# Optimization experiments

Hardware: AMD Instinct MI355X
Metric: run time of the kernel (lower is better)

Reference implementation:

```python
import jax, jax.numpy as jnp
import numpy as np

NUM_HEADS = 16
MASK_NEG = -66504.0  # matches IPEX causal mask fill value


def setup_inputs() -> dict:
    key = jax.random.key(0)
    ks = jax.random.split(key, 5)
    B, S, E = 1, 2048, 2048
    return {
        "hidden_states": jax.random.normal(ks[0], (B, S, E), dtype=jnp.float32),
        "q_wei": jax.random.normal(ks[1], (E, E), dtype=jnp.float32) * (E ** -0.5),
        "k_wei": jax.random.normal(ks[2], (E, E), dtype=jnp.float32) * (E ** -0.5),
        "v_wei": jax.random.normal(ks[3], (E, E), dtype=jnp.float32) * (E ** -0.5),
        "out_wei": jax.random.normal(ks[4], (E, E), dtype=jnp.float32) * (E ** -0.5),
    }


def reference(hidden_states, q_wei, k_wei, v_wei, out_wei):
    B, S, E = hidden_states.shape
    H = NUM_HEADS
    D = E // H
    # qkv_normal (row-major path): x @ W, [B,S,E]
    q = hidden_states @ q_wei
    k = hidden_states @ k_wei
    v = hidden_states @ v_wei
    # compute_qkv view + normal_combine permute -> [B,H,S,D]
    q = q.reshape(B, S, H, D).transpose(0, 2, 1, 3)
    k = k.reshape(B, S, H, D).transpose(0, 2, 1, 3)
    v = v.reshape(B, S, H, D).transpose(0, 2, 1, 3)
    # naive_self_attention: scores, causal mask add, THEN scale divide
    scores = jnp.einsum("bhqd,bhkd->bhqk", q, k)  # [B,H,S,S]
    causal = jnp.triu(jnp.full((S, S), MASK_NEG, dtype=scores.dtype), k=1)
    scores = scores + causal[None, None]
    scores = scores / jnp.sqrt(jnp.asarray(D, dtype=scores.dtype))
    probs = jax.nn.softmax(scores.astype(jnp.float32), axis=-1).astype(q.dtype)
    attn = jnp.einsum("bhqk,bhkd->bhqd", probs, v)  # [B,H,S,D]
    # merge heads and output projection
    attn = attn.transpose(0, 2, 1, 3).reshape(B, S, E)
    return attn @ out_wei
```

## Files before the change

### kernel.cpp

```cpp
#include <hip/hip_runtime.h>

#define F16 _Float16
typedef __attribute__((ext_vector_type(8))) _Float16 half8;
typedef __attribute__((ext_vector_type(4))) _Float16 half4;
typedef __attribute__((ext_vector_type(4))) float f32x4;

constexpr int S = 2048;
constexpr int E = 2048;
constexpr float MASK_NEG = -66504.0f;
constexpr float INV_SQRT_D = 0.08838834764831845f;
constexpr float MASK_SC = MASK_NEG * INV_SQRT_D;

__device__ __forceinline__ void gload16(const void* g, void* l) {
  __builtin_amdgcn_global_load_lds((const __attribute__((address_space(1))) void*)g,
                                   (__attribute__((address_space(3))) void*)l, 16, 0, 0);
}

__global__ __launch_bounds__(256) void cast_f32_f16_k(const float* __restrict__ x,
                                                      F16* __restrict__ y) {
  size_t i = ((size_t)blockIdx.x * 256 + threadIdx.x) * 8;
  float4 a = *(const float4*)(x + i);
  float4 b = *(const float4*)(x + i + 4);
  half8 h;
  h[0] = (F16)a.x; h[1] = (F16)a.y; h[2] = (F16)a.z; h[3] = (F16)a.w;
  h[4] = (F16)b.x; h[5] = (F16)b.y; h[6] = (F16)b.z; h[7] = (F16)b.w;
  *(half8*)(y + i) = h;
}

__global__ __launch_bounds__(256) void transpose_cast2_k(const float* __restrict__ W0,
                                                         const float* __restrict__ W1,
                                                         F16* __restrict__ D0,
                                                         F16* __restrict__ D1) {
  const float* W = blockIdx.z ? W1 : W0;
  F16* Wt = blockIdx.z ? D1 : D0;
  __shared__ float tile[64][65];
  const int t = threadIdx.x;
  const int bx = blockIdx.x, by = blockIdx.y;
  {
    int r = t >> 4, c = (t & 15) << 2;
    const float* src = W + (size_t)(by * 64 + r) * E + bx * 64 + c;
    #pragma unroll
    for (int i = 0; i < 4; ++i) {
      float4 v = *(const float4*)(src + (size_t)i * 16 * E);
      tile[r + i * 16][c + 0] = v.x; tile[r + i * 16][c + 1] = v.y;
      tile[r + i * 16][c + 2] = v.z; tile[r + i * 16][c + 3] = v.w;
    }
  }
  __syncthreads();
  {
    int r = t >> 2, c = (t & 3) << 4;
    half8 v0, v1;
    #pragma unroll
    for (int i = 0; i < 8; ++i) v0[i] = (F16)tile[c + i][r];
    #pragma unroll
    for (int i = 0; i < 8; ++i) v1[i] = (F16)tile[c + 8 + i][r];
    F16* dst = Wt + (size_t)(bx * 64 + r) * E + by * 64 + c;
    *(half8*)dst = v0;
    *(half8*)(dst + 8) = v1;
  }
}

template <int MODE>
__global__ __launch_bounds__(256, 2) void gemm_bt_k(const F16* __restrict__ A,
                                                    const F16* __restrict__ Bt,
                                                    void* __restrict__ C0v,
                                                    void* __restrict__ C1v) {
  constexpr int K = 2048, N = 2048;
  __shared__ F16 sA[64 * 64];
  __shared__ F16 sB[128 * 64];
  const int t = threadIdx.x;
  const int lane = t & 63, wave = t >> 6;
  const int wr = wave >> 1, wc = wave & 1;
  const int bm = blockIdx.y, bn = blockIdx.x;

  f32x4 acc[2][4];
  #pragma unroll
  for (int mi = 0; mi < 2; ++mi)
    #pragma unroll
    for (int ni = 0; ni < 4; ++ni) acc[mi][ni] = (f32x4){0.f, 0.f, 0.f, 0.f};

  const int rb = t >> 3;
  const int bofs = (t & 7) << 4;
  const int kOff = (bofs ^ ((rb & 7) << 4)) >> 1;
  const F16* aSrc = A + (size_t)(bm * 64 + rb) * K + kOff;
  const F16* bSrc = Bt + (size_t)(bn * 128 + rb) * K + kOff;
  F16* aDst = sA + t * 8;
  F16* bDst = sB + t * 8;

  for (int bk = 0; bk < K; bk += 64) {
    #pragma unroll
    for (int it = 0; it < 2; ++it)
      gload16(aSrc + (size_t)it * 32 * K + bk, aDst + it * 2048);
    #pragma unroll
    for (int it = 0; it < 4; ++it)
      gload16(bSrc + (size_t)it * 32 * K + bk, bDst + it * 2048);
    __syncthreads();
    #pragma unroll
    for (int kk = 0; kk < 2; ++kk) {
      half8 af[2], bf[4];
      const int kb = kk * 64 + ((lane >> 4) << 4);
      #pragma unroll
      for (int i = 0; i < 2; ++i) {
        const int ra = wr * 32 + i * 16 + (lane & 15);
        af[i] = *(const half8*)((const char*)sA + ra * 128 + (kb ^ ((ra & 7) << 4)));
      }
      #pragma unroll
      for (int i = 0; i < 4; ++i) {
        const int rn = wc * 64 + i * 16 + (lane & 15);
        bf[i] = *(const half8*)((const char*)sB + rn * 128 + (kb ^ ((rn & 7) << 4)));
      }
      #pragma unroll
      for (int mi = 0; mi < 2; ++mi)
        #pragma unroll
        for (int ni = 0; ni < 4; ++ni)
          acc[mi][ni] = __builtin_amdgcn_mfma_f32_16x16x32_f16(af[mi], bf[ni], acc[mi][ni], 0, 0, 0);
    }
    __syncthreads();
  }

  const float scale = (MODE == 1 && bn < 16) ? INV_SQRT_D : 1.0f;
  void* Cv = (MODE == 1 && bn >= 16) ? C1v : C0v;
  const int cb = (MODE == 1 ? (bn & 15) : bn) * 128;

  #pragma unroll
  for (int mi = 0; mi < 2; ++mi) {
    const int r0 = bm * 64 + wr * 32 + mi * 16 + ((lane >> 4) << 2);
    #pragma unroll
    for (int ni = 0; ni < 4; ++ni) {
      const int c = cb + wc * 64 + ni * 16 + (lane & 15);
      #pragma unroll
      for (int j = 0; j < 4; ++j) {
        if (MODE == 2)
          ((float*)Cv)[(size_t)(r0 + j) * N + c] = acc[mi][ni][j];
        else
          ((F16*)Cv)[(size_t)(r0 + j) * N + c] = (F16)(acc[mi][ni][j] * scale);
      }
    }
  }
}

__global__ __launch_bounds__(256, 2) void attn_fwd_k(const F16* __restrict__ Q,
                                                     const F16* __restrict__ Km,
                                                     const F16* __restrict__ Vt,
                                                     F16* __restrict__ O) {
  __shared__ F16 sK[2][64 * 128];
  __shared__ F16 sV[2][128 * 64];
  __shared__ F16 sP[4][16 * 64];
  const int t = threadIdx.x, lane = t & 63, w = t >> 6;
  const int h = blockIdx.x & 15;
  const int bq = blockIdx.x >> 4;
  const int qt = (bq < 16) ? (31 - bq) : (bq - 16);
  const int qrow0 = qt * 64 + w * 16;
  const int g = lane >> 4;
  const int myq = qrow0 + (lane & 15);

  half8 qf[4];
  {
    const F16* qp = Q + (size_t)myq * E + h * 128 + (g << 3);
    #pragma unroll
    for (int kd = 0; kd < 4; ++kd) qf[kd] = *(const half8*)(qp + kd * 32);
  }

  f32x4 oacc[8];
  #pragma unroll
  for (int i = 0; i < 8; ++i) oacc[i] = (f32x4){0.f, 0.f, 0.f, 0.f};
  float mrun = -3e38f, lrun = 0.f;

  const int rk = t >> 4;
  const int kcol = (((t & 15) << 4) ^ ((rk & 15) << 4)) >> 1;
  const int rv = t >> 3;
  const int vcol = (((t & 7) << 4) ^ ((rv & 7) << 4)) >> 1;
  const F16* kBase = Km + (size_t)rk * E + h * 128 + kcol;
  const F16* vBase = Vt + (size_t)(h * 128 + rv) * S + vcol;
  F16* myP = (F16*)sP[w];

  auto stage = [&](int kt, int b) {
    const F16* kSrc = kBase + (size_t)kt * 64 * E;
    const F16* vSrc = vBase + kt * 64;
    #pragma unroll
    for (int it = 0; it < 4; ++it) {
      gload16(kSrc + (size_t)it * 16 * E, &sK[b][t * 8 + it * 2048]);
      gload16(vSrc + (size_t)it * 32 * S, &sV[b][t * 8 + it * 2048]);
    }
  };

  stage(0, 0);
  const int nt = qt + 1;

  for (int kt = 0; kt < nt; ++kt) {
    __syncthreads();
    if (kt + 1 < nt) stage(kt + 1, (kt + 1) & 1);
    const char* bK = (const char*)sK[kt & 1];
    const char* bV = (const char*)sV[kt & 1];

    f32x4 sacc[4];
    #pragma unroll
    for (int i = 0; i < 4; ++i) sacc[i] = (f32x4){0.f, 0.f, 0.f, 0.f};
    __builtin_amdgcn_s_setprio(1);
    #pragma unroll
    for (int kd = 0; kd < 4; ++kd) {
      const int kb = kd * 64 + (g << 4);
      #pragma unroll
      for (int ni = 0; ni < 4; ++ni) {
        const int rn = ni * 16 + (lane & 15);
        half8 kf = *(const half8*)(bK + rn * 256 + (kb ^ ((rn & 15) << 4)));
        sacc[ni] = __builtin_amdgcn_mfma_f32_16x16x32_f16(kf, qf[kd], sacc[ni], 0, 0, 0);
      }
    }
    __builtin_amdgcn_s_setprio(0);

    const bool diag = (kt == nt - 1);
    const int kv0 = kt * 64 + g * 4;
    float mx = -3e38f;
    #pragma unroll
    for (int ni = 0; ni < 4; ++ni) {
      #pragma unroll
      for (int j = 0; j < 4; ++j) {
        float s = sacc[ni][j];
        if (diag && (kv0 + ni * 16 + j) > myq) s += MASK_SC;
        sacc[ni][j] = s;
        mx = fmaxf(mx, s);
      }
    }
    mx = fmaxf(mx, __shfl_xor(mx, 16));
    mx = fmaxf(mx, __shfl_xor(mx, 32));

    if (__any(mx > mrun + 8.0f)) {
      const float mnew = fmaxf(mrun, mx);
      const float sc = __expf(mrun - mnew);
      float rs = 0.f;
      #pragma unroll
      for (int ni = 0; ni < 4; ++ni)
        #pragma unroll
        for (int j = 0; j < 4; ++j) {
          const float p = __expf(sacc[ni][j] - mnew);
          sacc[ni][j] = p;
          rs += p;
        }
      rs += __shfl_xor(rs, 16);
      rs += __shfl_xor(rs, 32);
      lrun = lrun * sc + rs;
      mrun = mnew;
      #pragma unroll
      for (int df = 0; df < 8; ++df)
        #pragma unroll
        for (int j = 0; j < 4; ++j) oacc[df][j] *= sc;
    } else {
      float rs = 0.f;
      #pragma unroll
      for (int ni = 0; ni < 4; ++ni)
        #pragma unroll
        for (int j = 0; j < 4; ++j) {
          const float p = __expf(sacc[ni][j] - mrun);
          sacc[ni][j] = p;
          rs += p;
        }
      rs += __shfl_xor(rs, 16);
      rs += __shfl_xor(rs, 32);
      lrun += rs;
    }

    {
      char* rowp = (char*)myP + (lane & 15) * 128;
      const int swz = ((lane & 15) & 7) << 4;
      #pragma unroll
      for (int ni = 0; ni < 4; ++ni) {
        half4 pk;
        #pragma unroll
        for (int j = 0; j < 4; ++j) pk[j] = (F16)sacc[ni][j];
        *(half4*)(rowp + ((ni * 32 + g * 8) ^ swz)) = pk;
      }
    }

    __builtin_amdgcn_s_setprio(1);
    #pragma unroll
    for (int kk = 0; kk < 2; ++kk) {
      const int kb = kk * 64 + (g << 4);
      const int ra = lane & 15;
      half8 pa = *(const half8*)((const char*)myP + ra * 128 + (kb ^ ((ra & 7) << 4)));
      #pragma unroll
      for (int df = 0; df < 8; ++df) {
        const int rd = df * 16 + (lane & 15);
        half8 vf = *(const half8*)(bV + rd * 128 + (kb ^ ((rd & 7) << 4)));
        oacc[df] = __builtin_amdgcn_mfma_f32_16x16x32_f16(vf, pa, oacc[df], 0, 0, 0);
      }
    }
    __builtin_amdgcn_s_setprio(0);
  }

  const float inv = 1.0f / lrun;
  F16* orow = O + (size_t)myq * E + h * 128;
  #pragma unroll
  for (int df = 0; df < 8; ++df) {
    half4 ov;
    #pragma unroll
    for (int j = 0; j < 4; ++j) ov[j] = (F16)(oacc[df][j] * inv);
    *(half4*)(orow + df * 16 + g * 4) = ov;
  }
}

extern "C" void kernel_launch(void* const* d_in, const int* in_sizes, int n_in,
                              void* d_out, int out_size, void* d_ws, size_t ws_size,
                              hipStream_t stream) {
  const float* X  = (const float*)d_in[0];
  const float* Wq = (const float*)d_in[1];
  const float* Wk = (const float*)d_in[2];
  const float* Wv = (const float*)d_in[3];
  const float* Wo = (const float*)d_in[4];
  float* out = (float*)d_out;

  const size_t MAT = (size_t)2048 * 2048;
  F16* Xh  = (F16*)d_ws;
  F16* Wt0 = Xh + MAT;
  F16* Wt1 = Wt0 + MAT;
  F16* Qh  = Wt1 + MAT;
  F16* Kh  = Qh + MAT;
  F16* Vh  = Kh + MAT;

  dim3 b256(256);
  cast_f32_f16_k<<<dim3(MAT / 2048), b256, 0, stream>>>(X, Xh);

  transpose_cast2_k<<<dim3(32, 32, 2), b256, 0, stream>>>(Wq, Wk, Wt0, Wt1);
  gemm_bt_k<1><<<dim3(32, 32), b256, 0, stream>>>(Xh, Wt0, Qh, Kh);

  transpose_cast2_k<<<dim3(32, 32, 2), b256, 0, stream>>>(Wv, Wo, Wt0, Wt1);
  gemm_bt_k<0><<<dim3(16, 32), b256, 0, stream>>>(Wt0, Xh, Vh, nullptr);

  attn_fwd_k<<<dim3(512), b256, 0, stream>>>(Qh, Kh, Vh, Xh);

  gemm_bt_k<2><<<dim3(16, 32), b256, 0, stream>>>(Xh, Wt1, out, nullptr);
}
```

Before: 178.9 us.

## Split attention KV range across two blocks with 128-row query tiles and merge

The attention kernel now gives each wave 32 query rows (two 16-row MFMA tiles sharing each K/V fragment load). Each 128-row query tile's causal KV range is split into two halves handled by separate blocks, with balanced pairing. Partial outputs and running max/sum go to scratch (reusing the output buffer and the workspace), and a new merge kernel combines them before the output projection. This doubles K/V reuse per LDS read and balances causal work, at the cost of an extra kernel, partial-output traffic and higher register pressure.

```diff
diff --git a/kernel.cpp b/kernel.cpp
--- a/kernel.cpp
+++ b/kernel.cpp
@@ -142,29 +142,40 @@
 __global__ __launch_bounds__(256, 2) void attn_fwd_k(const F16* __restrict__ Q,
                                                      const F16* __restrict__ Km,
                                                      const F16* __restrict__ Vt,
-                                                     F16* __restrict__ O) {
+                                                     F16* __restrict__ Opart,
+                                                     float* __restrict__ mlArr) {
   __shared__ F16 sK[2][64 * 128];
   __shared__ F16 sV[2][128 * 64];
-  __shared__ F16 sP[4][16 * 64];
+  __shared__ F16 sP[4][32 * 64];
   const int t = threadIdx.x, lane = t & 63, w = t >> 6;
-  const int h = blockIdx.x & 15;
-  const int bq = blockIdx.x >> 4;
-  const int qt = (bq < 16) ? (31 - bq) : (bq - 16);
-  const int qrow0 = qt * 64 + w * 16;
-  const int g = lane >> 4;
-  const int myq = qrow0 + (lane & 15);
-
-  half8 qf[4];
+  const int c = blockIdx.x & 255;
+  const int sp = blockIdx.x >> 8;
+  const int h = c & 15;
+  const int qi = c >> 4;
+  const int qt = sp ? (15 - qi) : qi;
+  const int qrow0 = qt * 128 + w * 32;
+  const int l15 = lane & 15, g = lane >> 4;
+  const int q0 = qrow0 + l15;
+  const int q1 = qrow0 + 16 + l15;
+
+  half8 qf0[4], qf1[4];
   {
-    const F16* qp = Q + (size_t)myq * E + h * 128 + (g << 3);
-    #pragma unroll
-    for (int kd = 0; kd < 4; ++kd) qf[kd] = *(const half8*)(qp + kd * 32);
-  }
-
-  f32x4 oacc[8];
-  #pragma unroll
-  for (int i = 0; i < 8; ++i) oacc[i] = (f32x4){0.f, 0.f, 0.f, 0.f};
-  float mrun = -3e38f, lrun = 0.f;
+    const F16* qp0 = Q + (size_t)q0 * E + h * 128 + (g << 3);
+    const F16* qp1 = Q + (size_t)q1 * E + h * 128 + (g << 3);
+    #pragma unroll
+    for (int kd = 0; kd < 4; ++kd) {
+      qf0[kd] = *(const half8*)(qp0 + kd * 32);
+      qf1[kd] = *(const half8*)(qp1 + kd * 32);
+    }
+  }
+
+  f32x4 oacc0[8], oacc1[8];
+  #pragma unroll
+  for (int i = 0; i < 8; ++i) {
+    oacc0[i] = (f32x4){0.f, 0.f, 0.f, 0.f};
+    oacc1[i] = (f32x4){0.f, 0.f, 0.f, 0.f};
+  }
+  float m0r = -3e38f, l0r = 0.f, m1r = -3e38f, l1r = 0.f;
 
   const int rk = t >> 4;
   const int kcol = (((t & 15) << 4) ^ ((rk & 15) << 4)) >> 1;
@@ -184,91 +195,108 @@
     }
   };
 
-  stage(0, 0);
-  const int nt = qt + 1;
-
-  for (int kt = 0; kt < nt; ++kt) {
+  const int kb0 = sp * (qt + 1), kb1 = kb0 + qt + 1;
+  stage(kb0, kb0 & 1);
+
+  for (int kt = kb0; kt < kb1; ++kt) {
     __syncthreads();
-    if (kt + 1 < nt) stage(kt + 1, (kt + 1) & 1);
+    if (kt + 1 < kb1) stage(kt + 1, (kt + 1) & 1);
+    if (kt * 64 > qrow0 + 31) continue;
     const char* bK = (const char*)sK[kt & 1];
     const char* bV = (const char*)sV[kt & 1];
 
-    f32x4 sacc[4];
-    #pragma unroll
-    for (int i = 0; i < 4; ++i) sacc[i] = (f32x4){0.f, 0.f, 0.f, 0.f};
+    f32x4 sa0[4], sa1[4];
+    #pragma unroll
+    for (int i = 0; i < 4; ++i) {
+      sa0[i] = (f32x4){0.f, 0.f, 0.f, 0.f};
+      sa1[i] = (f32x4){0.f, 0.f, 0.f, 0.f};
+    }
     __builtin_amdgcn_s_setprio(1);
     #pragma unroll
     for (int kd = 0; kd < 4; ++kd) {
       const int kb = kd * 64 + (g << 4);
       #pragma unroll
       for (int ni = 0; ni < 4; ++ni) {
-        const int rn = ni * 16 + (lane & 15);
+        const int rn = ni * 16 + l15;
         half8 kf = *(const half8*)(bK + rn * 256 + (kb ^ ((rn & 15) << 4)));
-        sacc[ni] = __builtin_amdgcn_mfma_f32_16x16x32_f16(kf, qf[kd], sacc[ni], 0, 0, 0);
+        sa0[ni] = __builtin_amdgcn_mfma_f32_16x16x32_f16(kf, qf0[kd], sa0[ni], 0, 0, 0);
+        sa1[ni] = __builtin_amdgcn_mfma_f32_16x16x32_f16(kf, qf1[kd], sa1[ni], 0, 0, 0);
       }
     }
     __builtin_amdgcn_s_setprio(0);
 
-    const bool diag = (kt == nt - 1);
+    const bool diag = (kt * 64 + 63 > qrow0);
     const int kv0 = kt * 64 + g * 4;
-    float mx = -3e38f;
+    float mx0 = -3e38f, mx1 = -3e38f;
     #pragma unroll
     for (int ni = 0; ni < 4; ++ni) {
       #pragma unroll
       for (int j = 0; j < 4; ++j) {
-        float s = sacc[ni][j];
-        if (diag && (kv0 + ni * 16 + j) > myq) s += MASK_SC;
-        sacc[ni][j] = s;
-        mx = fmaxf(mx, s);
-      }
-    }
-    mx = fmaxf(mx, __shfl_xor(mx, 16));
-    mx = fmaxf(mx, __shfl_xor(mx, 32));
-
-    if (__any(mx > mrun + 8.0f)) {
-      const float mnew = fmaxf(mrun, mx);
-      const float sc = __expf(mrun - mnew);
-      float rs = 0.f;
+        const int kv = kv0 + ni * 16 + j;
+        float s0 = sa0[ni][j], s1 = sa1[ni][j];
+        if (diag && kv > q0) s0 += MASK_SC;
+        if (diag && kv > q1) s1 += MASK_SC;
+        sa0[ni][j] = s0; sa1[ni][j] = s1;
+        mx0 = fmaxf(mx0, s0); mx1 = fmaxf(mx1, s1);
+      }
+    }
+    mx0 = fmaxf(mx0, __shfl_xor(mx0, 16));
+    mx0 = fmaxf(mx0, __shfl_xor(mx0, 32));
+    mx1 = fmaxf(mx1, __shfl_xor(mx1, 16));
+    mx1 = fmaxf(mx1, __shfl_xor(mx1, 32));
+
+    if (__any((mx0 > m0r + 8.0f) || (mx1 > m1r + 8.0f))) {
+      const float mn0 = fmaxf(m0r, mx0), mn1 = fmaxf(m1r, mx1);
+      const float sc0 = __expf(m0r - mn0), sc1 = __expf(m1r - mn1);
+      float rs0 = 0.f, rs1 = 0.f;
       #pragma unroll
       for (int ni = 0; ni < 4; ++ni)
         #pragma unroll
         for (int j = 0; j < 4; ++j) {
-          const float p = __expf(sacc[ni][j] - mnew);
-          sacc[ni][j] = p;
-          rs += p;
+          const float p0 = __expf(sa0[ni][j] - mn0);
+          const float p1 = __expf(sa1[ni][j] - mn1);
+          sa0[ni][j] = p0; sa1[ni][j] = p1;
+          rs0 += p0; rs1 += p1;
         }
-      rs += __shfl_xor(rs, 16);
-      rs += __shfl_xor(rs, 32);
-      lrun = lrun * sc + rs;
-      mrun = mnew;
+      rs0 += __shfl_xor(rs0, 16); rs0 += __shfl_xor(rs0, 32);
+      rs1 += __shfl_xor(rs1, 16); rs1 += __shfl_xor(rs1, 32);
+      l0r = l0r * sc0 + rs0; l1r = l1r * sc1 + rs1;
+      m0r = mn0; m1r = mn1;
       #pragma unroll
       for (int df = 0; df < 8; ++df)
         #pragma unroll
-        for (int j = 0; j < 4; ++j) oacc[df][j] *= sc;
+        for (int j = 0; j < 4; ++j) {
+          oacc0[df][j] *= sc0;
+          oacc1[df][j] *= sc1;
+        }
     } else {
-      float rs = 0.f;
+      float rs0 = 0.f, rs1 = 0.f;
       #pragma unroll
       for (int ni = 0; ni < 4; ++ni)
         #pragma unroll
         for (int j = 0; j < 4; ++j) {
-          const float p = __expf(sacc[ni][j] - mrun);
-          sacc[ni][j] = p;
-          rs += p;
+          const float p0 = __expf(sa0[ni][j] - m0r);
+          const float p1 = __expf(sa1[ni][j] - m1r);
+          sa0[ni][j] = p0; sa1[ni][j] = p1;
+          rs0 += p0; rs1 += p1;
         }
-      rs += __shfl_xor(rs, 16);
-      rs += __shfl_xor(rs, 32);
-      lrun += rs;
+      rs0 += __shfl_xor(rs0, 16); rs0 += __shfl_xor(rs0, 32);
+      rs1 += __shfl_xor(rs1, 16); rs1 += __shfl_xor(rs1, 32);
+      l0r += rs0; l1r += rs1;
     }
 
     {
-      char* rowp = (char*)myP + (lane & 15) * 128;
-      const int swz = ((lane & 15) & 7) << 4;
+      char* rp0 = (char*)myP + l15 * 128;
+      char* rp1 = (char*)myP + (16 + l15) * 128;
+      const int sz0 = (l15 & 7) << 4;
+      const int sz1 = ((16 + l15) & 7) << 4;
       #pragma unroll
       for (int ni = 0; ni < 4; ++ni) {
-        half4 pk;
-        #pragma unroll
-        for (int j = 0; j < 4; ++j) pk[j] = (F16)sacc[ni][j];
-        *(half4*)(rowp + ((ni * 32 + g * 8) ^ swz)) = pk;
+        half4 p0, p1;
+        #pragma unroll
+        for (int j = 0; j < 4; ++j) { p0[j] = (F16)sa0[ni][j]; p1[j] = (F16)sa1[ni][j]; }
+        *(half4*)(rp0 + ((ni * 32 + g * 8) ^ sz0)) = p0;
+        *(half4*)(rp1 + ((ni * 32 + g * 8) ^ sz1)) = p1;
       }
     }
 
@@ -276,27 +304,62 @@
     #pragma unroll
     for (int kk = 0; kk < 2; ++kk) {
       const int kb = kk * 64 + (g << 4);
-      const int ra = lane & 15;
-      half8 pa = *(const half8*)((const char*)myP + ra * 128 + (kb ^ ((ra & 7) << 4)));
+      half8 pa0 = *(const half8*)((const char*)myP + l15 * 128 + (kb ^ ((l15 & 7) << 4)));
+      half8 pa1 = *(const half8*)((const char*)myP + (16 + l15) * 128 + (kb ^ (((16 + l15) & 7) << 4)));
       #pragma unroll
       for (int df = 0; df < 8; ++df) {
-        const int rd = df * 16 + (lane & 15);
+        const int rd = df * 16 + l15;
         half8 vf = *(const half8*)(bV + rd * 128 + (kb ^ ((rd & 7) << 4)));
-        oacc[df] = __builtin_amdgcn_mfma_f32_16x16x32_f16(vf, pa, oacc[df], 0, 0, 0);
+        oacc0[df] = __builtin_amdgcn_mfma_f32_16x16x32_f16(vf, pa0, oacc0[df], 0, 0, 0);
+        oacc1[df] = __builtin_amdgcn_mfma_f32_16x16x32_f16(vf, pa1, oacc1[df], 0, 0, 0);
       }
     }
     __builtin_amdgcn_s_setprio(0);
   }
 
-  const float inv = 1.0f / lrun;
-  F16* orow = O + (size_t)myq * E + h * 128;
+  const float inv0 = (l0r > 0.f) ? 1.0f / l0r : 0.f;
+  const float inv1 = (l1r > 0.f) ? 1.0f / l1r : 0.f;
+  const int row0 = (sp * 16 + h) * 2048 + q0;
+  const int row1 = (sp * 16 + h) * 2048 + q1;
+  F16* op0 = Opart + ((size_t)row0 << 7);
+  F16* op1 = Opart + ((size_t)row1 << 7);
   #pragma unroll
   for (int df = 0; df < 8; ++df) {
-    half4 ov;
-    #pragma unroll
-    for (int j = 0; j < 4; ++j) ov[j] = (F16)(oacc[df][j] * inv);
-    *(half4*)(orow + df * 16 + g * 4) = ov;
-  }
+    half4 o0, o1;
+    #pragma unroll
+    for (int j = 0; j < 4; ++j) {
+      o0[j] = (F16)(oacc0[df][j] * inv0);
+      o1[j] = (F16)(oacc1[df][j] * inv1);
+    }
+    *(half4*)(op0 + df * 16 + g * 4) = o0;
+    *(half4*)(op1 + df * 16 + g * 4) = o1;
+  }
+  if (g == 0) {
+    mlArr[row0] = m0r;          mlArr[row1] = m1r;
+    mlArr[65536 + row0] = l0r;  mlArr[65536 + row1] = l1r;
+  }
+}
+
+__global__ __launch_bounds__(256) void merge_k(const F16* __restrict__ Opart,
+                                               const float* __restrict__ mlArr,
+                                               F16* __restrict__ Om) {
+  const int tid = blockIdx.x * 256 + threadIdx.x;
+  const int row = tid >> 4;
+  const int d0 = (tid & 15) << 3;
+  const int h = row >> 11, q = row & 2047;
+  const float m0 = mlArr[row],          l0 = mlArr[65536 + row];
+  const float m1 = mlArr[32768 + row],  l1 = mlArr[98304 + row];
+  const float mm = fmaxf(m0, m1);
+  const float w0 = l0 * __expf(m0 - mm);
+  const float w1 = l1 * __expf(m1 - mm);
+  const float inv = 1.0f / (w0 + w1);
+  half8 a = *(const half8*)(Opart + ((size_t)row << 7) + d0);
+  half8 b = *(const half8*)(Opart + ((size_t)(32768 + row) << 7) + d0);
+  half8 o;
+  #pragma unroll
+  for (int j = 0; j < 8; ++j)
+    o[j] = (F16)((((float)a[j]) * w0 + ((float)b[j]) * w1) * inv);
+  *(half8*)(Om + (size_t)q * E + h * 128 + d0) = o;
 }
 
 extern "C" void kernel_launch(void* const* d_in, const int* in_sizes, int n_in,
@@ -316,6 +379,8 @@
   F16* Qh  = Wt1 + MAT;
   F16* Kh  = Qh + MAT;
   F16* Vh  = Kh + MAT;
+  float* mlArr = (float*)d_ws;
+  F16* Opart = (F16*)d_out;
 
   dim3 b256(256);
   cast_f32_f16_k<<<dim3(MAT / 2048), b256, 0, stream>>>(X, Xh);
@@ -326,7 +391,9 @@
   transpose_cast2_k<<<dim3(32, 32, 2), b256, 0, stream>>>(Wv, Wo, Wt0, Wt1);
   gemm_bt_k<0><<<dim3(16, 32), b256, 0, stream>>>(Wt0, Xh, Vh, nullptr);
 
-  attn_fwd_k<<<dim3(512), b256, 0, stream>>>(Qh, Kh, Vh, Xh);
-
-  gemm_bt_k<2><<<dim3(16, 32), b256, 0, stream>>>(Xh, Wt1, out, nullptr);
-}
+  attn_fwd_k<<<dim3(512), b256, 0, stream>>>(Qh, Kh, Vh, Opart, mlArr);
+
+  merge_k<<<dim3(2048), b256, 0, stream>>>(Opart, mlArr, Qh);
+
+  gemm_bt_k<2><<<dim3(16, 32), b256, 0, stream>>>(Qh, Wt1, out, nullptr);
+}
```

Result: slower. 198.6 us (+11.0%).
